# Kernel optimization log

Measured on AMD Instinct MI355X. Metric: run time of the kernel, lower is better.

Reference implementation:

```python
import jax, jax.numpy as jnp
import numpy as np

D = 1024
H = 16
DH = D // H  # 64
B = 2
T = 2048
GN_EPS = 0.00064


def setup_inputs() -> dict:
    key = jax.random.key(0)
    ks = jax.random.split(key, 16)
    def w(k):
        return jax.random.normal(k, (D, D), dtype=jnp.float32) * 0.02  # torch Linear weight [out,in]
    inp = {
        "x": jax.random.normal(ks[0], (B, T, D), dtype=jnp.float32),
        "ddlerp_w": w(ks[1]),
        "mix_r": jnp.full((D,), 0.5, dtype=jnp.float32),
        "mix_k": jnp.full((D,), 0.5, dtype=jnp.float32),
        "mix_v": jnp.full((D,), 0.5, dtype=jnp.float32),
        "mix_g": jnp.full((D,), 0.5, dtype=jnp.float32),
        "mix_w": jnp.full((D,), 0.5, dtype=jnp.float32),
        "r_w": w(ks[2]),
        "k_w": w(ks[3]),
        "v_w": w(ks[4]),
        "g_w": w(ks[5]),
        "w_w": w(ks[6]),
        "out_w": w(ks[7]),
        "gn_weight": jnp.ones((D,), dtype=jnp.float32),
        "gn_bias": jnp.zeros((D,), dtype=jnp.float32),
    }
    return inp


def _wkv_scan(r, k, v, w):
    # r,k,v,w: [B,T,H,Dh]. state: [B,H,Dh(k),Dh(v)]
    def step(state, inp):
        r_t, k_t, v_t, w_t = inp  # each [B,H,Dh]
        state = state * jnp.exp(w_t)[..., None] + k_t[..., None] * v_t[..., None, :]
        # torch: (state @ r[...,None]).squeeze(-1): contract v-dim of state with r
        o_t = jnp.einsum("bhkv,bhv->bhk", state, r_t)
        return state, o_t

    tm = lambda a: jnp.swapaxes(a, 0, 1)  # -> [T,B,H,Dh]
    state0 = jnp.zeros((r.shape[0], H, DH, DH), dtype=r.dtype)
    _, out = jax.lax.scan(step, state0, (tm(r), tm(k), tm(v), tm(w)))
    return jnp.swapaxes(out, 0, 1)  # [B,T,H,Dh]


def reference(x, ddlerp_w, mix_r, mix_k, mix_v, mix_g, mix_w,
              r_w, k_w, v_w, g_w, w_w, out_w, gn_weight, gn_bias):
    Bc, Tc, Dc = x.shape
    # token shift: F.pad(x, (0,0,1,-1)) -> prepend zero row, drop last
    x_shift = jnp.pad(x, ((0, 0), (1, 0), (0, 0)))[:, :Tc]
    dd = jax.nn.sigmoid(jnp.tanh(jnp.einsum("btd,ed->bte", x_shift, ddlerp_w)))

    def lerp(mix):
        m = mix + dd * (1.0 - mix)
        return x * m + x_shift * (1.0 - m)

    proj = lambda a, wgt: jnp.einsum("btd,ed->bte", a, wgt)
    r = proj(lerp(mix_r), r_w)
    k = proj(lerp(mix_k), k_w)
    v = proj(lerp(mix_v), v_w)
    g = jax.nn.silu(proj(lerp(mix_g), g_w))
    w = -jax.nn.softplus(-proj(lerp(mix_w), w_w)) - 0.5

    shape4 = (Bc, Tc, H, DH)
    out = _wkv_scan(r.reshape(shape4), k.reshape(shape4), v.reshape(shape4), w.reshape(shape4))

    # GroupNorm(n_heads, embed_dim, eps=0.00064) per (b,t) row
    mu = out.mean(axis=-1, keepdims=True)
    var = out.var(axis=-1, keepdims=True)
    out = (out - mu) / jnp.sqrt(var + GN_EPS)
    out = out * gn_weight.reshape(H, DH) + gn_bias.reshape(H, DH)
    out = out.reshape(Bc, Tc, Dc)

    return jnp.einsum("btd,ed->bte", out * g, out_w)
```

## Files before the change

kernel.cpp:

```cpp
#include <hip/hip_runtime.h>
#include <math.h>

typedef _Float16 h16;
typedef _Float16 h16x4 __attribute__((ext_vector_type(4)));
typedef _Float16 h16x8 __attribute__((ext_vector_type(8)));
typedef float    f32x4 __attribute__((ext_vector_type(4)));

#define Bsz 2
#define Tsz 2048
#define Dsz 1024
#define Hn  16
#define DH  64
#define NC  32
#define NCSH 5
#define CL  (Tsz/NC)
#define TS  16
#define NTL (CL/TS)
#define LP  68

__global__ void prep(const float* __restrict__ s0, const float* __restrict__ s1,
                     const float* __restrict__ s2, const float* __restrict__ s3,
                     const float* __restrict__ s4, const float* __restrict__ s5,
                     const float* __restrict__ s6, h16* __restrict__ dst,
                     const float* __restrict__ x, h16* __restrict__ xs) {
    int blk = blockIdx.x;
    if (blk < 7 * 512) {
        int seg = blk >> 9;
        int li  = ((blk & 511) << 8) + threadIdx.x;
        const float* sp;
        switch (seg) {
            case 0: sp = s0; break; case 1: sp = s1; break; case 2: sp = s2; break;
            case 3: sp = s3; break; case 4: sp = s4; break; case 5: sp = s5; break;
            default: sp = s6; break;
        }
        size_t e = (size_t)li * 8;
        f32x4 a = *(const f32x4*)(sp + e);
        f32x4 b = *(const f32x4*)(sp + e + 4);
        h16x8 o;
        #pragma unroll
        for (int j = 0; j < 4; ++j) { o[j] = (h16)a[j]; o[j + 4] = (h16)b[j]; }
        *(h16x8*)(dst + (size_t)seg * 1048576 + e) = o;
    } else {
        int li = ((blk - 7 * 512) << 8) + threadIdx.x;
        size_t e = (size_t)li * 8;
        int tok = (int)(e >> 10);
        int t   = tok & (Tsz - 1);
        h16x8 o;
        if (t > 0) {
            f32x4 a = *(const f32x4*)(x + e - Dsz);
            f32x4 b = *(const f32x4*)(x + e - Dsz + 4);
            #pragma unroll
            for (int j = 0; j < 4; ++j) { o[j] = (h16)a[j]; o[j + 4] = (h16)b[j]; }
        } else {
            #pragma unroll
            for (int j = 0; j < 8; ++j) o[j] = (h16)0.f;
        }
        *(h16x8*)(xs + e) = o;
    }
}

#define BK 32

__device__ __forceinline__ void gld16(const void* g, void* l) {
    __builtin_amdgcn_global_load_lds(
        (const __attribute__((address_space(1))) void*)g,
        (__attribute__((address_space(3))) void*)l, 16, 0, 0);
}

struct GemmCtx {
    f32x4 acc[4][4];
    int bm, bn, lane, wave, wm, wn;
};

__device__ __forceinline__ void gemm_kloop(GemmCtx& cx, const h16* __restrict__ A,
                                           const h16* __restrict__ W) {
    __shared__ h16 As[5][4096];
    __shared__ h16 Bs[5][4096];
    const int tid  = threadIdx.x;
    const int lane = tid & 63;
    const int wave = tid >> 6;
    cx.lane = lane; cx.wave = wave;
    cx.wm = (wave >> 1) * 64;
    cx.wn = (wave & 1) * 64;
    const int lin = blockIdx.y * 8 + blockIdx.x;
    const int g8  = lin & 7, sq = lin >> 3;
    cx.bm = (g8 * 4 + (sq >> 3)) * 128;
    cx.bn = (sq & 7) * 128;
    const int K = 1024;

    #pragma unroll
    for (int a = 0; a < 4; ++a)
        #pragma unroll
        for (int b = 0; b < 4; ++b) cx.acc[a][b] = (f32x4)(0.f);

    const int srow = (wave << 4) + (lane >> 2);
    const int scol = (((lane & 3) ^ ((lane >> 3) & 3)) << 3);
    const h16* gA0 = A + (size_t)(cx.bm + srow) * K + scol;
    const h16* gA1 = gA0 + (size_t)64 * K;
    const h16* gB0 = W + (size_t)(cx.bn + srow) * K + scol;
    const h16* gB1 = gB0 + (size_t)64 * K;

    const int pcq = (lane >> 4) ^ ((lane >> 1) & 3);
    const int fro = (lane & 15) * BK + pcq * 8;

    auto stage = [&](int b, int k0) {
        gld16(gA0 + k0, &As[b][wave * 512]);
        gld16(gA1 + k0, &As[b][2048 + wave * 512]);
        gld16(gB0 + k0, &Bs[b][wave * 512]);
        gld16(gB1 + k0, &Bs[b][2048 + wave * 512]);
    };
    auto compute = [&](int b) {
        const h16* as = As[b]; const h16* bs = Bs[b];
        h16x8 af[4], bfr[4];
        #pragma unroll
        for (int mi = 0; mi < 4; ++mi)
            af[mi] = *(const h16x8*)(as + (cx.wm + mi * 16) * BK + fro);
        #pragma unroll
        for (int ni = 0; ni < 4; ++ni)
            bfr[ni] = *(const h16x8*)(bs + (cx.wn + ni * 16) * BK + fro);
        __builtin_amdgcn_s_setprio(1);
        #pragma unroll
        for (int mi = 0; mi < 4; ++mi)
            #pragma unroll
            for (int ni = 0; ni < 4; ++ni)
                cx.acc[mi][ni] = __builtin_amdgcn_mfma_f32_16x16x32_f16(
                    af[mi], bfr[ni], cx.acc[mi][ni], 0, 0, 0);
        __builtin_amdgcn_s_setprio(0);
    };

    stage(0, 0);
    stage(1, BK);
    stage(2, 2 * BK);
    stage(3, 3 * BK);
    #pragma unroll
    for (int t = 0; t < 32; ++t) {
        if (t <= 28)      { asm volatile("s_waitcnt vmcnt(12)" ::: "memory"); }
        else if (t == 29) { asm volatile("s_waitcnt vmcnt(8)"  ::: "memory"); }
        else if (t == 30) { asm volatile("s_waitcnt vmcnt(4)"  ::: "memory"); }
        else              { asm volatile("s_waitcnt vmcnt(0)"  ::: "memory"); }
        __builtin_amdgcn_sched_barrier(0);
        __builtin_amdgcn_s_barrier();
        __builtin_amdgcn_sched_barrier(0);
        if (t + 4 < 32) stage((t + 4) % 5, (t + 4) * BK);
        compute(t % 5);
    }
}

template <typename OT>
__device__ __forceinline__ void gemm_body(const h16* __restrict__ A,
                                          const h16* __restrict__ W,
                                          OT* __restrict__ C, int epi) {
    GemmCtx cx;
    gemm_kloop(cx, A, W);
    const int colb = cx.bn + cx.wn + (cx.lane & 15);
    const int rowb = cx.bm + cx.wm + (cx.lane >> 4) * 4;
    #pragma unroll
    for (int mi = 0; mi < 4; ++mi)
        #pragma unroll
        for (int ni = 0; ni < 4; ++ni)
            #pragma unroll
            for (int j = 0; j < 4; ++j) {
                float y = cx.acc[mi][ni][j];
                if (epi == 2)      { y = y / (1.f + __expf(-y)); }
                else if (epi == 3) { y = 0.60653065971263342f / (1.f + __expf(-y)); }
                C[(size_t)(rowb + mi * 16 + j) * 1024 + colb + ni * 16] = (OT)y;
            }
}

__global__ __launch_bounds__(256) void gemm_bt_f(const h16* __restrict__ A,
                                                 const h16* __restrict__ W,
                                                 float* __restrict__ C, int epi) {
    gemm_body<float>(A, W, C, epi);
}

__global__ __launch_bounds__(256) void gemm_ddlerp(const h16* __restrict__ A,
                                                   const h16* __restrict__ W,
                                                   const float* __restrict__ x,
                                                   const float* __restrict__ mr,
                                                   const float* __restrict__ mk,
                                                   const float* __restrict__ mv,
                                                   const float* __restrict__ mg,
                                                   const float* __restrict__ mw,
                                                   h16* __restrict__ ar, h16* __restrict__ ak,
                                                   h16* __restrict__ av, h16* __restrict__ ag,
                                                   h16* __restrict__ aw) {
    GemmCtx cx;
    gemm_kloop(cx, A, W);
    const int colb = cx.bn + cx.wn + (cx.lane & 15);
    const int rowb = cx.bm + cx.wm + (cx.lane >> 4) * 4;
    #pragma unroll
    for (int mi = 0; mi < 4; ++mi)
        #pragma unroll
        for (int j = 0; j < 4; ++j) {
            int m = rowb + mi * 16 + j;
            int t = m & (Tsz - 1);
            #pragma unroll
            for (int ni = 0; ni < 4; ++ni) {
                int d = colb + ni * 16;
                size_t e = (size_t)m * 1024 + d;
                float y  = cx.acc[mi][ni][j];
                float th = 1.f - 2.f / (__expf(2.f * y) + 1.f);
                float dv = 1.f / (1.f + __expf(-th));
                float xv  = x[e];
                float xsv = (t > 0) ? x[e - Dsz] : 0.f;
                float dxx = xv - xsv;
                float m0 = mr[d], m1 = mk[d], m2 = mv[d], m3 = mg[d], m4 = mw[d];
                ar[e] = (h16)(xsv + dxx * (m0 + dv * (1.f - m0)));
                ak[e] = (h16)(xsv + dxx * (m1 + dv * (1.f - m1)));
                av[e] = (h16)(xsv + dxx * (m2 + dv * (1.f - m2)));
                ag[e] = (h16)(xsv + dxx * (m3 + dv * (1.f - m3)));
                aw[e] = (h16)(xsv + dxx * (m4 + dv * (1.f - m4)));
            }
        }
}

__global__ __launch_bounds__(256) void gemm5(const h16* __restrict__ A0, const h16* __restrict__ A1,
                                             const h16* __restrict__ A2, const h16* __restrict__ A3,
                                             const h16* __restrict__ A4, const h16* __restrict__ Wb,
                                             h16* __restrict__ C0, h16* __restrict__ C1,
                                             h16* __restrict__ C2, h16* __restrict__ C3,
                                             h16* __restrict__ C4) {
    int z = blockIdx.z;
    const h16* A; h16* C; int epi;
    switch (z) {
        case 0: A = A0; C = C0; epi = 0; break;
        case 1: A = A1; C = C1; epi = 0; break;
        case 2: A = A2; C = C2; epi = 0; break;
        case 3: A = A3; C = C3; epi = 2; break;
        default: A = A4; C = C4; epi = 3; break;
    }
    gemm_body<h16>(A, Wb + (size_t)(z + 1) * 1048576, C, epi);
}

__device__ __forceinline__ void cvt16(const h16x8 u0, const h16x8 u1,
                                      f32x4& t0, f32x4& t1, f32x4& t2, f32x4& t3) {
    #pragma unroll
    for (int j = 0; j < 4; ++j) {
        t0[j] = (float)u0[j];     t1[j] = (float)u0[j + 4];
        t2[j] = (float)u1[j];     t3[j] = (float)u1[j + 4];
    }
}

__global__ __launch_bounds__(256) void wkv_pass1(const h16* __restrict__ kk,
                                                 const h16* __restrict__ vv,
                                                 const h16* __restrict__ ew,
                                                 h16* __restrict__ Abuf,
                                                 float* __restrict__ Pbuf) {
    __shared__ float lds[2][3][TS][LP];
    int blk = blockIdx.x;
    int bh = blk >> NCSH, c = blk & (NC - 1);
    int b = bh >> 4, h = bh & 15;
    int tid = threadIdx.x;
    int i = tid >> 2, q = tid & 3, j0 = q * 16;
    int w = tid >> 6, idx = tid & 63;
    int ss = idx >> 2, qq = idx & 3;
    const h16* sarr = (w == 0) ? ew : (w == 1) ? kk : vv;

    float st[16];
    #pragma unroll
    for (int jj = 0; jj < 16; ++jj) st[jj] = 0.f;
    float pp = 1.f;

    size_t cbase = ((size_t)b * Tsz + (size_t)c * CL) * Dsz + h * DH;

    if (w < 3) {
        const h16x8* g = (const h16x8*)(sarr + cbase + (size_t)ss * Dsz + qq * 16);
        h16x8 u0 = g[0], u1 = g[1];
        f32x4 t0, t1, t2, t3;
        cvt16(u0, u1, t0, t1, t2, t3);
        f32x4* d = (f32x4*)&lds[0][w][ss][qq * 16];
        d[0] = t0; d[1] = t1; d[2] = t2; d[3] = t3;
    }
    __syncthreads();

    for (int tl = 0; tl < NTL; ++tl) {
        int cur = tl & 1;
        h16x8 u0, u1;
        bool pf = (tl + 1 < NTL) && (w < 3);
        if (pf) {
            const h16x8* g = (const h16x8*)(sarr + cbase + (size_t)(tl + 1) * TS * Dsz
                                            + (size_t)ss * Dsz + qq * 16);
            u0 = g[0]; u1 = g[1];
        }
        #pragma unroll 4
        for (int s = 0; s < TS; ++s) {
            float ewi = lds[cur][0][s][i];
            float ki  = lds[cur][1][s][i];
            const float* vrow = &lds[cur][2][s][0];
            f32x4 v0 = *(const f32x4*)(vrow + j0);
            f32x4 v1 = *(const f32x4*)(vrow + j0 + 4);
            f32x4 v2 = *(const f32x4*)(vrow + j0 + 8);
            f32x4 v3 = *(const f32x4*)(vrow + j0 + 12);
            #pragma unroll
            for (int jj = 0; jj < 4; ++jj) {
                st[jj]      = fmaf(st[jj],      ewi, ki * v0[jj]);
                st[jj + 4]  = fmaf(st[jj + 4],  ewi, ki * v1[jj]);
                st[jj + 8]  = fmaf(st[jj + 8],  ewi, ki * v2[jj]);
                st[jj + 12] = fmaf(st[jj + 12], ewi, ki * v3[jj]);
            }
            pp *= ewi;
        }
        if (pf) {
            f32x4 t0, t1, t2, t3;
            cvt16(u0, u1, t0, t1, t2, t3);
            f32x4* d = (f32x4*)&lds[cur ^ 1][w][ss][qq * 16];
            d[0] = t0; d[1] = t1; d[2] = t2; d[3] = t3;
        }
        __syncthreads();
    }

    size_t ob = (size_t)blk * 4096 + (size_t)i * 64 + j0;
    h16x8 s0, s1;
    #pragma unroll
    for (int jj = 0; jj < 8; ++jj) { s0[jj] = (h16)st[jj]; s1[jj] = (h16)st[jj + 8]; }
    *(h16x8*)(Abuf + ob)     = s0;
    *(h16x8*)(Abuf + ob + 8) = s1;
    if (q == 0) Pbuf[blk * 64 + i] = pp;
}

__global__ __launch_bounds__(256) void wkv_combine(h16* __restrict__ AS,
                                                   const float* __restrict__ Pbuf) {
    int bh = blockIdx.x >> 2, jq = blockIdx.x & 3;
    int tid = threadIdx.x;
    int i = tid >> 2, sc = tid & 3;
    int off = i * 64 + jq * 16 + sc * 4;
    float s[4] = {0.f, 0.f, 0.f, 0.f};
    size_t base = (size_t)(bh * NC) * 4096 + off;
    h16x4 a0 = *(const h16x4*)(AS + base);
    float p0 = Pbuf[bh * NC * 64 + i];
    h16x4 a1 = *(const h16x4*)(AS + base + 4096);
    float p1 = Pbuf[(bh * NC + 1) * 64 + i];
    for (int c = 0; c < NC; ++c) {
        h16x4 a2{}; float p2 = 0.f;
        if (c + 2 < NC) {
            a2 = *(const h16x4*)(AS + base + 2 * 4096);
            p2 = Pbuf[(bh * NC + c + 2) * 64 + i];
        }
        h16x4 so;
        #pragma unroll
        for (int j = 0; j < 4; ++j) so[j] = (h16)s[j];
        *(h16x4*)(AS + base) = so;
        #pragma unroll
        for (int j = 0; j < 4; ++j) s[j] = fmaf(s[j], p0, (float)a0[j]);
        a0 = a1; p0 = p1; a1 = a2; p1 = p2;
        base += 4096;
    }
}

__global__ __launch_bounds__(256) void wkv_pass2(const h16* __restrict__ rr,
                                                 const h16* __restrict__ kk,
                                                 const h16* __restrict__ vv,
                                                 const h16* __restrict__ ew,
                                                 const h16* __restrict__ Sbuf,
                                                 h16* __restrict__ o) {
    __shared__ float lds[2][4][TS][LP];
    int blk = blockIdx.x;
    int bh = blk >> NCSH, c = blk & (NC - 1);
    int b = bh >> 4, h = bh & 15;
    int tid = threadIdx.x;
    int i = tid >> 2, q = tid & 3, j0 = q * 16;
    int w = tid >> 6, idx = tid & 63;
    int ss = idx >> 2, qq = idx & 3;
    const h16* sarr = (w == 0) ? ew : (w == 1) ? kk : (w == 2) ? vv : rr;

    float st[16];
    {
        size_t ob = (size_t)blk * 4096 + (size_t)i * 64 + j0;
        h16x8 s0 = *(const h16x8*)(Sbuf + ob);
        h16x8 s1 = *(const h16x8*)(Sbuf + ob + 8);
        #pragma unroll
        for (int jj = 0; jj < 8; ++jj) { st[jj] = (float)s0[jj]; st[jj + 8] = (float)s1[jj]; }
    }

    size_t cbase = ((size_t)b * Tsz + (size_t)c * CL) * Dsz + h * DH;

    {
        const h16x8* g = (const h16x8*)(sarr + cbase + (size_t)ss * Dsz + qq * 16);
        h16x8 u0 = g[0], u1 = g[1];
        f32x4 t0, t1, t2, t3;
        cvt16(u0, u1, t0, t1, t2, t3);
        f32x4* d = (f32x4*)&lds[0][w][ss][qq * 16];
        d[0] = t0; d[1] = t1; d[2] = t2; d[3] = t3;
    }
    __syncthreads();

    for (int tl = 0; tl < NTL; ++tl) {
        int cur = tl & 1;
        h16x8 u0, u1;
        bool pf = (tl + 1 < NTL);
        if (pf) {
            const h16x8* g = (const h16x8*)(sarr + cbase + (size_t)(tl + 1) * TS * Dsz
                                            + (size_t)ss * Dsz + qq * 16);
            u0 = g[0]; u1 = g[1];
        }
        size_t gt = cbase + (size_t)tl * TS * Dsz;
        #pragma unroll 4
        for (int s = 0; s < TS; ++s) {
            float ewi = lds[cur][0][s][i];
            float ki  = lds[cur][1][s][i];
            const float* vrow = &lds[cur][2][s][0];
            const float* rrow = &lds[cur][3][s][0];
            f32x4 v0 = *(const f32x4*)(vrow + j0);
            f32x4 v1 = *(const f32x4*)(vrow + j0 + 4);
            f32x4 v2 = *(const f32x4*)(vrow + j0 + 8);
            f32x4 v3 = *(const f32x4*)(vrow + j0 + 12);
            f32x4 r0 = *(const f32x4*)(rrow + j0);
            f32x4 r1 = *(const f32x4*)(rrow + j0 + 4);
            f32x4 r2 = *(const f32x4*)(rrow + j0 + 8);
            f32x4 r3 = *(const f32x4*)(rrow + j0 + 12);
            float po = 0.f;
            #pragma unroll
            for (int jj = 0; jj < 4; ++jj) {
                st[jj]      = fmaf(st[jj],      ewi, ki * v0[jj]);
                st[jj + 4]  = fmaf(st[jj + 4],  ewi, ki * v1[jj]);
                st[jj + 8]  = fmaf(st[jj + 8],  ewi, ki * v2[jj]);
                st[jj + 12] = fmaf(st[jj + 12], ewi, ki * v3[jj]);
                po = fmaf(st[jj],      r0[jj], po);
                po = fmaf(st[jj + 4],  r1[jj], po);
                po = fmaf(st[jj + 8],  r2[jj], po);
                po = fmaf(st[jj + 12], r3[jj], po);
            }
            po += __shfl_xor(po, 1, 64);
            po += __shfl_xor(po, 2, 64);
            if (q == 0) o[gt + (size_t)s * Dsz + i] = (h16)po;
        }
        if (pf) {
            f32x4 t0, t1, t2, t3;
            cvt16(u0, u1, t0, t1, t2, t3);
            f32x4* d = (f32x4*)&lds[cur ^ 1][w][ss][qq * 16];
            d[0] = t0; d[1] = t1; d[2] = t2; d[3] = t3;
        }
        __syncthreads();
    }
}

__global__ __launch_bounds__(256) void gn_gate(const h16* __restrict__ o,
                                               const h16* __restrict__ g,
                                               const float* __restrict__ gnw,
                                               const float* __restrict__ gnb,
                                               h16* __restrict__ out) {
    int wave = threadIdx.x >> 6, lane = threadIdx.x & 63;
    int grp = blockIdx.x * 4 + wave;
    int h = grp & 15;
    float val = (float)o[(size_t)grp * 64 + lane];
    float s = val, s2 = val * val;
    #pragma unroll
    for (int m = 1; m < 64; m <<= 1) {
        s  += __shfl_xor(s, m, 64);
        s2 += __shfl_xor(s2, m, 64);
    }
    float mean = s * (1.f / 64.f);
    float var  = s2 * (1.f / 64.f) - mean * mean;
    float y = (val - mean) * rsqrtf(var + 0.00064f);
    int d = h * 64 + lane;
    y = y * gnw[d] + gnb[d];
    y *= (float)g[(size_t)grp * 64 + lane];
    out[(size_t)grp * 64 + lane] = (h16)y;
}

extern "C" void kernel_launch(void* const* d_in, const int* in_sizes, int n_in,
                              void* d_out, int out_size, void* d_ws, size_t ws_size,
                              hipStream_t stream) {
    const float* x      = (const float*)d_in[0];
    const float* ddw    = (const float*)d_in[1];
    const float* mix_r  = (const float*)d_in[2];
    const float* mix_k  = (const float*)d_in[3];
    const float* mix_v  = (const float*)d_in[4];
    const float* mix_g  = (const float*)d_in[5];
    const float* mix_w  = (const float*)d_in[6];
    const float* r_w    = (const float*)d_in[7];
    const float* k_w    = (const float*)d_in[8];
    const float* v_w    = (const float*)d_in[9];
    const float* g_w    = (const float*)d_in[10];
    const float* w_w    = (const float*)d_in[11];
    const float* out_w  = (const float*)d_in[12];
    const float* gnw    = (const float*)d_in[13];
    const float* gnb    = (const float*)d_in[14];

    char* wsb = (char*)d_ws;
    const size_t MB = 1 << 20;
    h16*   wb    = (h16*)  (wsb);
    h16*   xs    = (h16*)  (wsb + 14 * MB);
    h16*   a_r   = (h16*)  (wsb + 22 * MB);
    h16*   a_k   = (h16*)  (wsb + 30 * MB);
    h16*   a_v   = (h16*)  (wsb + 38 * MB);
    h16*   a_g   = (h16*)  (wsb + 46 * MB);
    h16*   a_w   = (h16*)  (wsb + 54 * MB);
    h16*   rb    = (h16*)  (wsb + 62 * MB);
    h16*   kb    = (h16*)  (wsb + 70 * MB);
    h16*   vb    = (h16*)  (wsb + 78 * MB);
    h16*   gb    = (h16*)  (wsb + 86 * MB);
    h16*   ewb   = (h16*)  (wsb + 94 * MB);
    h16*   obuf  = (h16*)  (wsb + 102 * MB);
    h16*   gated = (h16*)  (wsb + 110 * MB);
    h16*   Abuf  = (h16*)  (wsb + 22 * MB);
    float* Pbuf  = (float*)(wsb + 31 * MB);

    prep<<<7 * 512 + 2048, 256, 0, stream>>>(ddw, r_w, k_w, v_w, g_w, w_w, out_w,
                                             wb, x, xs);
    dim3 gg(8, 32);
    gemm_ddlerp<<<gg, 256, 0, stream>>>(xs, wb, x, mix_r, mix_k, mix_v, mix_g, mix_w,
                                        a_r, a_k, a_v, a_g, a_w);
    dim3 gg5(8, 32, 5);
    gemm5<<<gg5, 256, 0, stream>>>(a_r, a_k, a_v, a_g, a_w, wb, rb, kb, vb, gb, ewb);
    wkv_pass1<<<32 * NC, 256, 0, stream>>>(kb, vb, ewb, Abuf, Pbuf);
    wkv_combine<<<32 * 4, 256, 0, stream>>>(Abuf, Pbuf);
    wkv_pass2<<<32 * NC, 256, 0, stream>>>(rb, kb, vb, ewb, Abuf, obuf);
    gn_gate<<<(int)((size_t)Bsz * Tsz * Hn / 4), 256, 0, stream>>>(obuf, gb, gnw, gnb, gated);
    gemm_bt_f<<<gg, 256, 0, stream>>>(gated, wb + 6 * 1048576, (float*)d_out, 0);
    (void)in_sizes; (void)n_in; (void)out_size; (void)ws_size;
}
```

Measured before the change: 193.7 us.

## Give gemm5 its own 256x128 tile kernel with triple-buffered LDS pipeline

Replaces the shared gemm_body call in the five-way projection GEMM with a dedicated body. It uses 256x128 block tiles, 8x4 MFMA fragments per wave, triple-buffered async global-to-LDS staging, grouped block ordering for L2 reuse, and setprio around the MFMA bursts. The grid halves in y to match the taller tiles. The goals are more reuse per load, better hiding of load latency, and fewer blocks. The cost is more accumulator registers and LDS per block (launch_bounds 256,2), which risks lower occupancy.

```diff
diff --git a/kernel.cpp b/kernel.cpp
--- a/kernel.cpp
+++ b/kernel.cpp
@@ -214,12 +214,15 @@
         }
 }
 
-__global__ __launch_bounds__(256) void gemm5(const h16* __restrict__ A0, const h16* __restrict__ A1,
-                                             const h16* __restrict__ A2, const h16* __restrict__ A3,
-                                             const h16* __restrict__ A4, const h16* __restrict__ Wb,
-                                             h16* __restrict__ C0, h16* __restrict__ C1,
-                                             h16* __restrict__ C2, h16* __restrict__ C3,
-                                             h16* __restrict__ C4) {
+__global__ __launch_bounds__(256, 2) void gemm5(
+        const h16* __restrict__ A0, const h16* __restrict__ A1,
+        const h16* __restrict__ A2, const h16* __restrict__ A3,
+        const h16* __restrict__ A4, const h16* __restrict__ Wb,
+        h16* __restrict__ C0, h16* __restrict__ C1,
+        h16* __restrict__ C2, h16* __restrict__ C3,
+        h16* __restrict__ C4) {
+    __shared__ h16 As[3][8192];
+    __shared__ h16 Bs[3][4096];
     int z = blockIdx.z;
     const h16* A; h16* C; int epi;
     switch (z) {
@@ -229,7 +232,86 @@
         case 3: A = A3; C = C3; epi = 2; break;
         default: A = A4; C = C4; epi = 3; break;
     }
-    gemm_body<h16>(A, Wb + (size_t)(z + 1) * 1048576, C, epi);
+    const h16* W = Wb + (size_t)(z + 1) * 1048576;
+
+    const int tid  = threadIdx.x;
+    const int lane = tid & 63;
+    const int wave = tid >> 6;
+    const int wr = (wave >> 1) * 128;
+    const int wc = (wave & 1) * 64;
+    const int lin = blockIdx.y * 8 + blockIdx.x;
+    const int g8  = lin & 7, sq = lin >> 3;
+    const int bm  = (g8 * 2 + (sq >> 3)) * 256;
+    const int bn  = (sq & 7) * 128;
+    const int K = 1024;
+
+    f32x4 acc[8][4];
+    #pragma unroll
+    for (int a = 0; a < 8; ++a)
+        #pragma unroll
+        for (int b = 0; b < 4; ++b) acc[a][b] = (f32x4)(0.f);
+
+    const int srow = (wave << 4) + (lane >> 2);
+    const int scol = (((lane & 3) ^ ((lane >> 3) & 3)) << 3);
+    const h16* gA = A + (size_t)bm * K + (size_t)srow * K + scol;
+    const h16* gB0 = W + (size_t)(bn + srow) * K + scol;
+    const h16* gB1 = gB0 + (size_t)64 * K;
+
+    const int pcq = (lane >> 4) ^ ((lane >> 1) & 3);
+    const int fro = (lane & 15) * BK + pcq * 8;
+
+    auto stage = [&](int b, int k0) {
+        #pragma unroll
+        for (int qg = 0; qg < 4; ++qg)
+            gld16(gA + (size_t)qg * 64 * K + k0, &As[b][qg * 2048 + wave * 512]);
+        gld16(gB0 + k0, &Bs[b][wave * 512]);
+        gld16(gB1 + k0, &Bs[b][2048 + wave * 512]);
+    };
+    auto compute = [&](int b) {
+        const h16* as = As[b]; const h16* bs = Bs[b];
+        h16x8 af[8], bfr[4];
+        #pragma unroll
+        for (int mi = 0; mi < 8; ++mi)
+            af[mi] = *(const h16x8*)(as + (wr + mi * 16) * BK + fro);
+        #pragma unroll
+        for (int ni = 0; ni < 4; ++ni)
+            bfr[ni] = *(const h16x8*)(bs + (wc + ni * 16) * BK + fro);
+        __builtin_amdgcn_s_setprio(1);
+        #pragma unroll
+        for (int mi = 0; mi < 8; ++mi)
+            #pragma unroll
+            for (int ni = 0; ni < 4; ++ni)
+                acc[mi][ni] = __builtin_amdgcn_mfma_f32_16x16x32_f16(
+                    af[mi], bfr[ni], acc[mi][ni], 0, 0, 0);
+        __builtin_amdgcn_s_setprio(0);
+    };
+
+    stage(0, 0);
+    stage(1, BK);
+    #pragma unroll
+    for (int t = 0; t < 32; ++t) {
+        if (t < 31) { asm volatile("s_waitcnt vmcnt(6)" ::: "memory"); }
+        else        { asm volatile("s_waitcnt vmcnt(0)" ::: "memory"); }
+        __builtin_amdgcn_sched_barrier(0);
+        __builtin_amdgcn_s_barrier();
+        __builtin_amdgcn_sched_barrier(0);
+        if (t + 2 < 32) stage((t + 2) % 3, (t + 2) * BK);
+        compute(t % 3);
+    }
+
+    const int colb = bn + wc + (lane & 15);
+    const int rowb = bm + wr + (lane >> 4) * 4;
+    #pragma unroll
+    for (int mi = 0; mi < 8; ++mi)
+        #pragma unroll
+        for (int ni = 0; ni < 4; ++ni)
+            #pragma unroll
+            for (int j = 0; j < 4; ++j) {
+                float y = acc[mi][ni][j];
+                if (epi == 2)      { y = y / (1.f + __expf(-y)); }
+                else if (epi == 3) { y = 0.60653065971263342f / (1.f + __expf(-y)); }
+                C[(size_t)(rowb + mi * 16 + j) * 1024 + colb + ni * 16] = (h16)y;
+            }
 }
 
 __device__ __forceinline__ void cvt16(const h16x8 u0, const h16x8 u1,
@@ -501,7 +583,7 @@
     dim3 gg(8, 32);
     gemm_ddlerp<<<gg, 256, 0, stream>>>(xs, wb, x, mix_r, mix_k, mix_v, mix_g, mix_w,
                                         a_r, a_k, a_v, a_g, a_w);
-    dim3 gg5(8, 32, 5);
+    dim3 gg5(8, 16, 5);
     gemm5<<<gg5, 256, 0, stream>>>(a_r, a_k, a_v, a_g, a_w, wb, rb, kb, vb, gb, ewb);
     wkv_pass1<<<32 * NC, 256, 0, stream>>>(kb, vb, ewb, Abuf, Pbuf);
     wkv_combine<<<32 * 4, 256, 0, stream>>>(Abuf, Pbuf);
```

Result: slower. 202.1 us (+4.3%).
